# Performance work log

Measured on AMD Instinct MI355X. Metric: run time of the kernel, lower is better.

## Reference

```python
import jax, jax.numpy as jnp
import numpy as np

N_HEADS = 16


def setup_inputs() -> dict:
    key = jax.random.key(0)
    k1, k2, k3 = jax.random.split(key, 3)
    B, T, D = 2, 2048, 1024
    x = jax.random.normal(k1, (B, T, D), dtype=jnp.float32)
    w_qkv = jax.random.normal(k2, (3 * D, D), dtype=jnp.float32) * 0.02
    w_proj = jax.random.normal(k3, (D, D), dtype=jnp.float32) * (0.02 / np.sqrt(24.0))
    return {"x": x, "w_qkv": w_qkv, "w_proj": w_proj}


def reference(x, w_qkv, w_proj):
    B, T, D = x.shape
    H = N_HEADS
    dh = D // H
    # qkv linear (no bias): x @ w_qkv.T -> [B, T, 3D]
    qkv = jnp.einsum('btd,ed->bte', x, w_qkv)
    q, k, v = jnp.split(qkv, 3, axis=-1)
    q = q.reshape(B, T, H, dh)
    k = k.reshape(B, T, H, dh)
    v = v.reshape(B, T, H, dh)
    # attention with materialized scores [B, H, T, S]
    scores = jnp.einsum('bthd,bshd->bhts', q, k) / jnp.sqrt(jnp.asarray(dh, x.dtype))
    attn = jax.nn.softmax(scores.astype(jnp.float32), axis=-1).astype(x.dtype)
    out = jnp.einsum('bhts,bshd->bthd', attn, v).reshape(B, T, D)
    # output projection (no bias)
    return jnp.einsum('btd,ed->bte', out, w_proj)
```

## Files before the change

### kernel.cpp

```cpp
#include <hip/hip_runtime.h>


typedef __attribute__((ext_vector_type(8))) short s8v;
typedef __attribute__((ext_vector_type(8))) unsigned short us8;
typedef __attribute__((ext_vector_type(4))) float f4v;
typedef __attribute__((ext_vector_type(16))) float f16v;

__device__ __forceinline__ unsigned short f2b(float f) {
    unsigned u = __builtin_bit_cast(unsigned, f);
    u += 0x7FFFu + ((u >> 16) & 1u);
    return (unsigned short)(u >> 16);
}
__device__ __forceinline__ unsigned packtrunc(float a, float b, unsigned sel) {
    unsigned r;
    asm("v_perm_b32 %0, %1, %2, %3"
        : "=v"(r)
        : "v"(__builtin_bit_cast(unsigned, b)), "v"(__builtin_bit_cast(unsigned, a)), "s"(sel));
    return r;
}

#if __has_builtin(__builtin_amdgcn_exp2f)
#define EXP2F(x) __builtin_amdgcn_exp2f(x)
#else
#define EXP2F(x) exp2f(x)
#endif

#define QSCALE 0.18033688011112042f

__global__ __launch_bounds__(256) void cvt_all(const float* __restrict__ x,
                                               const float* __restrict__ wq,
                                               const float* __restrict__ wp,
                                               unsigned short* __restrict__ xb,
                                               unsigned short* __restrict__ wqb,
                                               unsigned short* __restrict__ wpb) {
    const int nx = 4096 * 1024 / 4, nq = 3072 * 1024 / 4;
    int i = blockIdx.x * 256 + threadIdx.x;
    const float* s;
    unsigned short* d;
    int j;
    if (i < nx)           { s = x;  d = xb;  j = i; }
    else if (i < nx + nq) { s = wq; d = wqb; j = i - nx; }
    else                  { s = wp; d = wpb; j = i - nx - nq; }
    float4 v = ((const float4*)s)[j];
    ushort4 o;
    o.x = f2b(v.x); o.y = f2b(v.y); o.z = f2b(v.z); o.w = f2b(v.w);
    ((ushort4*)d)[j] = o;
}

#define GLD_LDS16(g, l)                                                                        \
    __builtin_amdgcn_global_load_lds((const __attribute__((address_space(1))) unsigned*)(g),   \
                                     (__attribute__((address_space(3))) unsigned*)(l), 16, 0, 0)

__global__ __launch_bounds__(256) void gemm_qkv(const unsigned short* __restrict__ A,
                                                const unsigned short* __restrict__ B,
                                                unsigned short* __restrict__ qkvb) {
    __shared__ unsigned short As[128][32];
    __shared__ unsigned short Bs[128][32];
    const int tid = threadIdx.x;
    const int l = tid & 63, w = tid >> 6;
    const int quad = l >> 4, ln = l & 15;
    const int m0 = blockIdx.y * 128, n0 = blockIdx.x * 128;
    const int wm = (w >> 1) * 64, wn = (w & 1) * 64;

    const f4v fz = {0.f, 0.f, 0.f, 0.f};
    f4v acc[4][4];
#pragma unroll
    for (int i = 0; i < 4; ++i)
#pragma unroll
        for (int j = 0; j < 4; ++j) acc[i][j] = fz;

    const int row0 = tid >> 2, kc = tid & 3;
    for (int k0 = 0; k0 < 1024; k0 += 32) {
        GLD_LDS16(A + (size_t)(m0 + row0) * 1024 + k0 + kc * 8, &As[row0][kc * 8]);
        GLD_LDS16(B + (size_t)(n0 + row0) * 1024 + k0 + kc * 8, &Bs[row0][kc * 8]);
        GLD_LDS16(A + (size_t)(m0 + row0 + 64) * 1024 + k0 + kc * 8, &As[row0 + 64][kc * 8]);
        GLD_LDS16(B + (size_t)(n0 + row0 + 64) * 1024 + k0 + kc * 8, &Bs[row0 + 64][kc * 8]);
        __syncthreads();
        s8v af[4], bf[4];
#pragma unroll
        for (int mt = 0; mt < 4; ++mt) af[mt] = *(const s8v*)&As[wm + mt * 16 + ln][quad * 8];
#pragma unroll
        for (int nt = 0; nt < 4; ++nt) bf[nt] = *(const s8v*)&Bs[wn + nt * 16 + ln][quad * 8];
#pragma unroll
        for (int mt = 0; mt < 4; ++mt)
#pragma unroll
            for (int nt = 0; nt < 4; ++nt)
                acc[mt][nt] = __builtin_amdgcn_mfma_f32_16x16x32_bf16(af[mt], bf[nt], acc[mt][nt], 0, 0, 0);
        __syncthreads();
    }

#pragma unroll
    for (int mt = 0; mt < 4; ++mt)
#pragma unroll
        for (int nt = 0; nt < 4; ++nt) {
            const int col = n0 + wn + nt * 16 + ln;
            const int row = m0 + wm + mt * 16 + quad * 4;
            const float sc = (col < 1024) ? QSCALE : 1.0f;
#pragma unroll
            for (int r = 0; r < 4; ++r)
                qkvb[(size_t)(row + r) * 3072 + col] = f2b(acc[mt][nt][r] * sc);
        }
}

__global__ __launch_bounds__(256) void vtrans(const unsigned short* __restrict__ qkvb,
                                              unsigned short* __restrict__ vtb) {
    __shared__ unsigned Ls[64][65];
    const int tid = threadIdx.x;
    const int t0 = blockIdx.x * 64, h = blockIdx.y, b = blockIdx.z;
#pragma unroll
    for (int it = 0; it < 2; ++it) {
        int idx = tid + it * 256;
        int r = idx >> 3, c8 = idx & 7;
        us8 v = *(const us8*)(qkvb + ((size_t)b * 2048 + t0 + r) * 3072 + 2048 + h * 64 + c8 * 8);
#pragma unroll
        for (int j = 0; j < 8; ++j) Ls[r][c8 * 8 + j] = v[j];
    }
    __syncthreads();
#pragma unroll
    for (int it = 0; it < 2; ++it) {
        int idx = tid + it * 256;
        int d = idx >> 3, tc = idx & 7;
        us8 o;
#pragma unroll
        for (int j = 0; j < 8; ++j) o[j] = (unsigned short)Ls[tc * 8 + j][d];
        *(us8*)(vtb + ((size_t)(b * 16 + h) * 64 + d) * 2048 + t0 + tc * 8) = o;
    }
}

__global__ __launch_bounds__(256) void gemm_proj(const unsigned short* __restrict__ A,
                                                 const unsigned short* __restrict__ B,
                                                 float* __restrict__ C) {
    __shared__ unsigned short As[128][32];
    __shared__ unsigned short Bs[64][32];
    const int tid = threadIdx.x;
    const int l = tid & 63, w = tid >> 6;
    const int quad = l >> 4, ln = l & 15;
    const int m0 = blockIdx.y * 128, n0 = blockIdx.x * 64;
    const int wm = w * 32;

    const f4v fz = {0.f, 0.f, 0.f, 0.f};
    f4v acc[2][4];
#pragma unroll
    for (int i = 0; i < 2; ++i)
#pragma unroll
        for (int j = 0; j < 4; ++j) acc[i][j] = fz;

    const int row0 = tid >> 2, kc = tid & 3;
    for (int k0 = 0; k0 < 1024; k0 += 32) {
        GLD_LDS16(A + (size_t)(m0 + row0) * 1024 + k0 + kc * 8, &As[row0][kc * 8]);
        GLD_LDS16(A + (size_t)(m0 + row0 + 64) * 1024 + k0 + kc * 8, &As[row0 + 64][kc * 8]);
        GLD_LDS16(B + (size_t)(n0 + row0) * 1024 + k0 + kc * 8, &Bs[row0][kc * 8]);
        __syncthreads();
        s8v af[2], bf[4];
#pragma unroll
        for (int mt = 0; mt < 2; ++mt) af[mt] = *(const s8v*)&As[wm + mt * 16 + ln][quad * 8];
#pragma unroll
        for (int nt = 0; nt < 4; ++nt) bf[nt] = *(const s8v*)&Bs[nt * 16 + ln][quad * 8];
#pragma unroll
        for (int mt = 0; mt < 2; ++mt)
#pragma unroll
            for (int nt = 0; nt < 4; ++nt)
                acc[mt][nt] = __builtin_amdgcn_mfma_f32_16x16x32_bf16(af[mt], bf[nt], acc[mt][nt], 0, 0, 0);
        __syncthreads();
    }

#pragma unroll
    for (int mt = 0; mt < 2; ++mt)
#pragma unroll
        for (int nt = 0; nt < 4; ++nt) {
            const int row = m0 + wm + mt * 16 + quad * 4;
            const int col = n0 + nt * 16 + ln;
#pragma unroll
            for (int r = 0; r < 4; ++r) C[(size_t)(row + r) * 1024 + col] = acc[mt][nt][r];
        }
}

__global__ __launch_bounds__(256) void attn_mfma(const unsigned short* __restrict__ qkvb,
                                                 const unsigned short* __restrict__ vtb,
                                                 unsigned short* __restrict__ attnb) {
    __shared__ unsigned short Ks[2][64][76];
    __shared__ unsigned short Vt[2][64][76];
    __shared__ unsigned short Ps[128][76];
    __shared__ float lred[128];

    const int tid = threadIdx.x;
    const int l = tid & 63, w = tid >> 6;
    const int m31 = l & 31, h2 = l >> 5;
    const int qw = w * 32;
    const int t0 = blockIdx.x * 128;
    const int hh = blockIdx.y, bb = blockIdx.z;
    const size_t rowbase = (size_t)bb * 2048;
    const unsigned sel = 0x07060302u;
    const unsigned short* Vg = vtb + (size_t)(bb * 16 + hh) * 64 * 2048;

#pragma unroll
    for (int it = 0; it < 4; ++it) {
        const int idx = tid + it * 256;
        const int qr = idx >> 3, qc = (idx & 7) * 8;
        *(us8*)&Ps[qr][qc] = *(const us8*)(qkvb + (rowbase + t0 + qr) * 3072 + hh * 64 + qc);
    }
    __syncthreads();
    s8v qf[4];
#pragma unroll
    for (int k4 = 0; k4 < 4; ++k4)
        qf[k4] = *(const s8v*)&Ps[qw + m31][k4 * 16 + h2 * 8];

    const int r0 = tid >> 3, c0 = (tid & 7) * 8;

    f16v zz;
#pragma unroll
    for (int i = 0; i < 16; ++i) zz[i] = 0.f;
    f16v oacc[2];
    oacc[0] = zz; oacc[1] = zz;
    float lsum = 0.f;

    us8 kreg0 = *(const us8*)(qkvb + (rowbase + r0) * 3072 + 1024 + hh * 64 + c0);
    us8 kreg1 = *(const us8*)(qkvb + (rowbase + r0 + 32) * 3072 + 1024 + hh * 64 + c0);
    us8 vreg0 = *(const us8*)(Vg + (size_t)r0 * 2048 + c0);
    us8 vreg1 = *(const us8*)(Vg + (size_t)(r0 + 32) * 2048 + c0);
    *(us8*)&Ks[0][r0][c0] = kreg0;
    *(us8*)&Ks[0][r0 + 32][c0] = kreg1;
    *(us8*)&Vt[0][r0][c0] = vreg0;
    *(us8*)&Vt[0][r0 + 32][c0] = vreg1;

    for (int i = 0; i < 32; ++i) {
        const int cur = i & 1;
        __syncthreads();

        if (i + 1 < 32) {
            const int sn = (i + 1) * 64;
            kreg0 = *(const us8*)(qkvb + (rowbase + sn + r0) * 3072 + 1024 + hh * 64 + c0);
            kreg1 = *(const us8*)(qkvb + (rowbase + sn + r0 + 32) * 3072 + 1024 + hh * 64 + c0);
            vreg0 = *(const us8*)(Vg + (size_t)r0 * 2048 + sn + c0);
            vreg1 = *(const us8*)(Vg + (size_t)(r0 + 32) * 2048 + sn + c0);
        }

        f16v sacc[2];
        sacc[0] = zz; sacc[1] = zz;
#pragma unroll
        for (int k4 = 0; k4 < 4; ++k4) {
#pragma unroll
            for (int st = 0; st < 2; ++st) {
                s8v kf = *(const s8v*)&Ks[cur][st * 32 + m31][k4 * 16 + h2 * 8];
                sacc[st] = __builtin_amdgcn_mfma_f32_32x32x16_bf16(kf, qf[k4], sacc[st], 0, 0, 0);
            }
        }

#pragma unroll
        for (int st = 0; st < 2; ++st)
#pragma unroll
            for (int g = 0; g < 4; ++g) {
                float p0 = EXP2F(sacc[st][g * 4 + 0]);
                float p1 = EXP2F(sacc[st][g * 4 + 1]);
                float p2 = EXP2F(sacc[st][g * 4 + 2]);
                float p3 = EXP2F(sacc[st][g * 4 + 3]);
                lsum += (p0 + p1) + (p2 + p3);
                uint2 pk;
                pk.x = packtrunc(p0, p1, sel);
                pk.y = packtrunc(p2, p3, sel);
                *(uint2*)&Ps[qw + m31][st * 32 + g * 8 + h2 * 4] = pk;
            }

#pragma unroll
        for (int k2 = 0; k2 < 4; ++k2) {
            s8v pf = *(const s8v*)&Ps[qw + m31][k2 * 16 + h2 * 8];
#pragma unroll
            for (int nt = 0; nt < 2; ++nt) {
                s8v vfr = *(const s8v*)&Vt[cur][nt * 32 + m31][k2 * 16 + h2 * 8];
                oacc[nt] = __builtin_amdgcn_mfma_f32_32x32x16_bf16(pf, vfr, oacc[nt], 0, 0, 0);
            }
        }

        if (i + 1 < 32) {
            *(us8*)&Ks[1 - cur][r0][c0] = kreg0;
            *(us8*)&Ks[1 - cur][r0 + 32][c0] = kreg1;
            *(us8*)&Vt[1 - cur][r0][c0] = vreg0;
            *(us8*)&Vt[1 - cur][r0 + 32][c0] = vreg1;
        }
    }

    lsum += __shfl_xor(lsum, 32, 64);
    lred[qw + m31] = lsum;
    float inv[16];
#pragma unroll
    for (int g = 0; g < 4; ++g)
#pragma unroll
        for (int r = 0; r < 4; ++r)
            inv[g * 4 + r] = 1.001955f / lred[qw + 8 * g + 4 * h2 + r];

#pragma unroll
    for (int nt = 0; nt < 2; ++nt)
#pragma unroll
        for (int g = 0; g < 4; ++g)
#pragma unroll
            for (int r = 0; r < 4; ++r) {
                const int qrow = 8 * g + 4 * h2 + r;
                float o = oacc[nt][g * 4 + r] * inv[g * 4 + r];
                attnb[(rowbase + t0 + qw + qrow) * 1024 + hh * 64 + nt * 32 + m31] = f2b(o);
            }
}

extern "C" void kernel_launch(void* const* d_in, const int* in_sizes, int n_in,
                              void* d_out, int out_size, void* d_ws, size_t ws_size,
                              hipStream_t stream) {
    const float* x      = (const float*)d_in[0];
    const float* w_qkv  = (const float*)d_in[1];
    const float* w_proj = (const float*)d_in[2];
    float* out = (float*)d_out;

    char* p = (char*)d_ws;
    unsigned short* xb    = (unsigned short*)p;  p += (size_t)4096 * 1024 * 2;
    unsigned short* wqb   = (unsigned short*)p;  p += (size_t)3072 * 1024 * 2;
    unsigned short* wpb   = (unsigned short*)p;  p += (size_t)1024 * 1024 * 2;
    unsigned short* qkvb  = (unsigned short*)p;  p += (size_t)4096 * 3072 * 2;
    unsigned short* vtb   = (unsigned short*)p;  p += (size_t)2 * 16 * 64 * 2048 * 2;
    unsigned short* attnb = (unsigned short*)p;  p += (size_t)4096 * 1024 * 2;

    cvt_all<<<8192, 256, 0, stream>>>(x, w_qkv, w_proj, xb, wqb, wpb);

    gemm_qkv<<<dim3(3072 / 128, 4096 / 128), 256, 0, stream>>>(xb, wqb, qkvb);

    vtrans<<<dim3(32, 16, 2), 256, 0, stream>>>(qkvb, vtb);

    attn_mfma<<<dim3(2048 / 128, 16, 2), 256, 0, stream>>>(qkvb, vtb, attnb);

    gemm_proj<<<dim3(1024 / 64, 4096 / 128), 256, 0, stream>>>(attnb, wpb, out);
}
```

Before: 189.0 us.

## Fuse V transpose into attention and widen GEMM K-tiles with XOR-swizzled LDS

The separate vtrans kernel and its vtb buffer are removed. The attention kernel now loads V rows straight from the qkv buffer and transposes them in registers before writing to LDS. Both GEMMs move from a 32-wide to a 64-wide K tile, with XOR-swizzled global-to-LDS placement to avoid bank conflicts and half as many barriers per K step. This saves a kernel launch and a round trip through global memory, but the attention loads become narrower 8-byte strided reads and the GEMMs use more LDS.

```diff
diff --git a/kernel.cpp b/kernel.cpp
--- a/kernel.cpp
+++ b/kernel.cpp
@@ -3,6 +3,7 @@
 
 typedef __attribute__((ext_vector_type(8))) short s8v;
 typedef __attribute__((ext_vector_type(8))) unsigned short us8;
+typedef __attribute__((ext_vector_type(4))) unsigned short us4;
 typedef __attribute__((ext_vector_type(4))) float f4v;
 typedef __attribute__((ext_vector_type(16))) float f16v;
 
@@ -54,8 +55,8 @@
 __global__ __launch_bounds__(256) void gemm_qkv(const unsigned short* __restrict__ A,
                                                 const unsigned short* __restrict__ B,
                                                 unsigned short* __restrict__ qkvb) {
-    __shared__ unsigned short As[128][32];
-    __shared__ unsigned short Bs[128][32];
+    __shared__ unsigned short As[128][64];
+    __shared__ unsigned short Bs[128][64];
     const int tid = threadIdx.x;
     const int l = tid & 63, w = tid >> 6;
     const int quad = l >> 4, ln = l & 15;
@@ -69,23 +70,32 @@
 #pragma unroll
         for (int j = 0; j < 4; ++j) acc[i][j] = fz;
 
-    const int row0 = tid >> 2, kc = tid & 3;
-    for (int k0 = 0; k0 < 1024; k0 += 32) {
-        GLD_LDS16(A + (size_t)(m0 + row0) * 1024 + k0 + kc * 8, &As[row0][kc * 8]);
-        GLD_LDS16(B + (size_t)(n0 + row0) * 1024 + k0 + kc * 8, &Bs[row0][kc * 8]);
-        GLD_LDS16(A + (size_t)(m0 + row0 + 64) * 1024 + k0 + kc * 8, &As[row0 + 64][kc * 8]);
-        GLD_LDS16(B + (size_t)(n0 + row0 + 64) * 1024 + k0 + kc * 8, &Bs[row0 + 64][kc * 8]);
-        __syncthreads();
-        s8v af[4], bf[4];
-#pragma unroll
-        for (int mt = 0; mt < 4; ++mt) af[mt] = *(const s8v*)&As[wm + mt * 16 + ln][quad * 8];
-#pragma unroll
-        for (int nt = 0; nt < 4; ++nt) bf[nt] = *(const s8v*)&Bs[wn + nt * 16 + ln][quad * 8];
-#pragma unroll
-        for (int mt = 0; mt < 4; ++mt)
-#pragma unroll
-            for (int nt = 0; nt < 4; ++nt)
-                acc[mt][nt] = __builtin_amdgcn_mfma_f32_16x16x32_bf16(af[mt], bf[nt], acc[mt][nt], 0, 0, 0);
+    const int srow = tid >> 3, sc8 = tid & 7;
+    const int gcol = ((sc8 ^ (srow & 7)) << 3);
+    const int koff0 = ((quad ^ (ln & 7)) << 3);
+    const int koff1 = (((4 + quad) ^ (ln & 7)) << 3);
+
+    for (int k0 = 0; k0 < 1024; k0 += 64) {
+#pragma unroll
+        for (int b = 0; b < 4; ++b) {
+            GLD_LDS16(A + (size_t)(m0 + srow + 32 * b) * 1024 + k0 + gcol, &As[srow + 32 * b][sc8 * 8]);
+            GLD_LDS16(B + (size_t)(n0 + srow + 32 * b) * 1024 + k0 + gcol, &Bs[srow + 32 * b][sc8 * 8]);
+        }
+        __syncthreads();
+#pragma unroll
+        for (int ks = 0; ks < 2; ++ks) {
+            const int ko = ks ? koff1 : koff0;
+            s8v af[4], bf[4];
+#pragma unroll
+            for (int mt = 0; mt < 4; ++mt) af[mt] = *(const s8v*)&As[wm + mt * 16 + ln][ko];
+#pragma unroll
+            for (int nt = 0; nt < 4; ++nt) bf[nt] = *(const s8v*)&Bs[wn + nt * 16 + ln][ko];
+#pragma unroll
+            for (int mt = 0; mt < 4; ++mt)
+#pragma unroll
+                for (int nt = 0; nt < 4; ++nt)
+                    acc[mt][nt] = __builtin_amdgcn_mfma_f32_16x16x32_bf16(af[mt], bf[nt], acc[mt][nt], 0, 0, 0);
+        }
         __syncthreads();
     }
 
@@ -102,36 +112,11 @@
         }
 }
 
-__global__ __launch_bounds__(256) void vtrans(const unsigned short* __restrict__ qkvb,
-                                              unsigned short* __restrict__ vtb) {
-    __shared__ unsigned Ls[64][65];
-    const int tid = threadIdx.x;
-    const int t0 = blockIdx.x * 64, h = blockIdx.y, b = blockIdx.z;
-#pragma unroll
-    for (int it = 0; it < 2; ++it) {
-        int idx = tid + it * 256;
-        int r = idx >> 3, c8 = idx & 7;
-        us8 v = *(const us8*)(qkvb + ((size_t)b * 2048 + t0 + r) * 3072 + 2048 + h * 64 + c8 * 8);
-#pragma unroll
-        for (int j = 0; j < 8; ++j) Ls[r][c8 * 8 + j] = v[j];
-    }
-    __syncthreads();
-#pragma unroll
-    for (int it = 0; it < 2; ++it) {
-        int idx = tid + it * 256;
-        int d = idx >> 3, tc = idx & 7;
-        us8 o;
-#pragma unroll
-        for (int j = 0; j < 8; ++j) o[j] = (unsigned short)Ls[tc * 8 + j][d];
-        *(us8*)(vtb + ((size_t)(b * 16 + h) * 64 + d) * 2048 + t0 + tc * 8) = o;
-    }
-}
-
 __global__ __launch_bounds__(256) void gemm_proj(const unsigned short* __restrict__ A,
                                                  const unsigned short* __restrict__ B,
                                                  float* __restrict__ C) {
-    __shared__ unsigned short As[128][32];
-    __shared__ unsigned short Bs[64][32];
+    __shared__ unsigned short As[128][64];
+    __shared__ unsigned short Bs[64][64];
     const int tid = threadIdx.x;
     const int l = tid & 63, w = tid >> 6;
     const int quad = l >> 4, ln = l & 15;
@@ -145,22 +130,33 @@
 #pragma unroll
         for (int j = 0; j < 4; ++j) acc[i][j] = fz;
 
-    const int row0 = tid >> 2, kc = tid & 3;
-    for (int k0 = 0; k0 < 1024; k0 += 32) {
-        GLD_LDS16(A + (size_t)(m0 + row0) * 1024 + k0 + kc * 8, &As[row0][kc * 8]);
-        GLD_LDS16(A + (size_t)(m0 + row0 + 64) * 1024 + k0 + kc * 8, &As[row0 + 64][kc * 8]);
-        GLD_LDS16(B + (size_t)(n0 + row0) * 1024 + k0 + kc * 8, &Bs[row0][kc * 8]);
-        __syncthreads();
-        s8v af[2], bf[4];
-#pragma unroll
-        for (int mt = 0; mt < 2; ++mt) af[mt] = *(const s8v*)&As[wm + mt * 16 + ln][quad * 8];
-#pragma unroll
-        for (int nt = 0; nt < 4; ++nt) bf[nt] = *(const s8v*)&Bs[nt * 16 + ln][quad * 8];
-#pragma unroll
-        for (int mt = 0; mt < 2; ++mt)
-#pragma unroll
-            for (int nt = 0; nt < 4; ++nt)
-                acc[mt][nt] = __builtin_amdgcn_mfma_f32_16x16x32_bf16(af[mt], bf[nt], acc[mt][nt], 0, 0, 0);
+    const int srow = tid >> 3, sc8 = tid & 7;
+    const int gcol = ((sc8 ^ (srow & 7)) << 3);
+    const int koff0 = ((quad ^ (ln & 7)) << 3);
+    const int koff1 = (((4 + quad) ^ (ln & 7)) << 3);
+
+    for (int k0 = 0; k0 < 1024; k0 += 64) {
+#pragma unroll
+        for (int b = 0; b < 4; ++b)
+            GLD_LDS16(A + (size_t)(m0 + srow + 32 * b) * 1024 + k0 + gcol, &As[srow + 32 * b][sc8 * 8]);
+#pragma unroll
+        for (int b = 0; b < 2; ++b)
+            GLD_LDS16(B + (size_t)(n0 + srow + 32 * b) * 1024 + k0 + gcol, &Bs[srow + 32 * b][sc8 * 8]);
+        __syncthreads();
+#pragma unroll
+        for (int ks = 0; ks < 2; ++ks) {
+            const int ko = ks ? koff1 : koff0;
+            s8v af[2], bf[4];
+#pragma unroll
+            for (int mt = 0; mt < 2; ++mt) af[mt] = *(const s8v*)&As[wm + mt * 16 + ln][ko];
+#pragma unroll
+            for (int nt = 0; nt < 4; ++nt) bf[nt] = *(const s8v*)&Bs[nt * 16 + ln][ko];
+#pragma unroll
+            for (int mt = 0; mt < 2; ++mt)
+#pragma unroll
+                for (int nt = 0; nt < 4; ++nt)
+                    acc[mt][nt] = __builtin_amdgcn_mfma_f32_16x16x32_bf16(af[mt], bf[nt], acc[mt][nt], 0, 0, 0);
+        }
         __syncthreads();
     }
 
@@ -176,7 +172,6 @@
 }
 
 __global__ __launch_bounds__(256) void attn_mfma(const unsigned short* __restrict__ qkvb,
-                                                 const unsigned short* __restrict__ vtb,
                                                  unsigned short* __restrict__ attnb) {
     __shared__ unsigned short Ks[2][64][76];
     __shared__ unsigned short Vt[2][64][76];
@@ -191,7 +186,6 @@
     const int hh = blockIdx.y, bb = blockIdx.z;
     const size_t rowbase = (size_t)bb * 2048;
     const unsigned sel = 0x07060302u;
-    const unsigned short* Vg = vtb + (size_t)(bb * 16 + hh) * 64 * 2048;
 
 #pragma unroll
     for (int it = 0; it < 4; ++it) {
@@ -206,6 +200,7 @@
         qf[k4] = *(const s8v*)&Ps[qw + m31][k4 * 16 + h2 * 8];
 
     const int r0 = tid >> 3, c0 = (tid & 7) * 8;
+    const int va = tid >> 4, vc = tid & 15;
 
     f16v zz;
 #pragma unroll
@@ -216,12 +211,19 @@
 
     us8 kreg0 = *(const us8*)(qkvb + (rowbase + r0) * 3072 + 1024 + hh * 64 + c0);
     us8 kreg1 = *(const us8*)(qkvb + (rowbase + r0 + 32) * 3072 + 1024 + hh * 64 + c0);
-    us8 vreg0 = *(const us8*)(Vg + (size_t)r0 * 2048 + c0);
-    us8 vreg1 = *(const us8*)(Vg + (size_t)(r0 + 32) * 2048 + c0);
+    us4 vreg[4];
+#pragma unroll
+    for (int j = 0; j < 4; ++j)
+        vreg[j] = *(const us4*)(qkvb + (rowbase + 4 * va + j) * 3072 + 2048 + hh * 64 + 4 * vc);
     *(us8*)&Ks[0][r0][c0] = kreg0;
     *(us8*)&Ks[0][r0 + 32][c0] = kreg1;
-    *(us8*)&Vt[0][r0][c0] = vreg0;
-    *(us8*)&Vt[0][r0 + 32][c0] = vreg1;
+#pragma unroll
+    for (int dd = 0; dd < 4; ++dd) {
+        unsigned lo = (unsigned)vreg[0][dd] | ((unsigned)vreg[1][dd] << 16);
+        unsigned hi = (unsigned)vreg[2][dd] | ((unsigned)vreg[3][dd] << 16);
+        uint2 pk2; pk2.x = lo; pk2.y = hi;
+        *(uint2*)&Vt[0][4 * vc + dd][4 * va] = pk2;
+    }
 
     for (int i = 0; i < 32; ++i) {
         const int cur = i & 1;
@@ -231,8 +233,9 @@
             const int sn = (i + 1) * 64;
             kreg0 = *(const us8*)(qkvb + (rowbase + sn + r0) * 3072 + 1024 + hh * 64 + c0);
             kreg1 = *(const us8*)(qkvb + (rowbase + sn + r0 + 32) * 3072 + 1024 + hh * 64 + c0);
-            vreg0 = *(const us8*)(Vg + (size_t)r0 * 2048 + sn + c0);
-            vreg1 = *(const us8*)(Vg + (size_t)(r0 + 32) * 2048 + sn + c0);
+#pragma unroll
+            for (int j = 0; j < 4; ++j)
+                vreg[j] = *(const us4*)(qkvb + (rowbase + sn + 4 * va + j) * 3072 + 2048 + hh * 64 + 4 * vc);
         }
 
         f16v sacc[2];
@@ -274,8 +277,13 @@
         if (i + 1 < 32) {
             *(us8*)&Ks[1 - cur][r0][c0] = kreg0;
             *(us8*)&Ks[1 - cur][r0 + 32][c0] = kreg1;
-            *(us8*)&Vt[1 - cur][r0][c0] = vreg0;
-            *(us8*)&Vt[1 - cur][r0 + 32][c0] = vreg1;
+#pragma unroll
+            for (int dd = 0; dd < 4; ++dd) {
+                unsigned lo = (unsigned)vreg[0][dd] | ((unsigned)vreg[1][dd] << 16);
+                unsigned hi = (unsigned)vreg[2][dd] | ((unsigned)vreg[3][dd] << 16);
+                uint2 pk2; pk2.x = lo; pk2.y = hi;
+                *(uint2*)&Vt[1 - cur][4 * vc + dd][4 * va] = pk2;
+            }
         }
     }
 
@@ -313,16 +321,13 @@
     unsigned short* wqb   = (unsigned short*)p;  p += (size_t)3072 * 1024 * 2;
     unsigned short* wpb   = (unsigned short*)p;  p += (size_t)1024 * 1024 * 2;
     unsigned short* qkvb  = (unsigned short*)p;  p += (size_t)4096 * 3072 * 2;
-    unsigned short* vtb   = (unsigned short*)p;  p += (size_t)2 * 16 * 64 * 2048 * 2;
     unsigned short* attnb = (unsigned short*)p;  p += (size_t)4096 * 1024 * 2;
 
     cvt_all<<<8192, 256, 0, stream>>>(x, w_qkv, w_proj, xb, wqb, wpb);
 
     gemm_qkv<<<dim3(3072 / 128, 4096 / 128), 256, 0, stream>>>(xb, wqb, qkvb);
 
-    vtrans<<<dim3(32, 16, 2), 256, 0, stream>>>(qkvb, vtb);
-
-    attn_mfma<<<dim3(2048 / 128, 16, 2), 256, 0, stream>>>(qkvb, vtb, attnb);
+    attn_mfma<<<dim3(2048 / 128, 16, 2), 256, 0, stream>>>(qkvb, attnb);
 
     gemm_proj<<<dim3(1024 / 64, 4096 / 128), 256, 0, stream>>>(attnb, wpb, out);
 }
```

Measured after the change: 188.7 us. No clear change (-0.2%).
